# Performance work log

Hardware: AMD Instinct MI355X
Metric: run time of the kernel (lower is better)

## Reference

```python
import jax, jax.numpy as jnp
import numpy as np

N_NODES = 50000
IN_DIM = 128
HIDDEN = 64
OUT_DIM = 3
HEADS1 = 4
NEG_SLOPE = 0.2
EPS = 1e-16


def _glorot(key, shape):
    fan_in, fan_out = shape[0], shape[-1]
    lim = (6.0 / (fan_in + fan_out)) ** 0.5
    return jax.random.uniform(key, shape, jnp.float32, -lim, lim)


def setup_inputs() -> dict:
    key = jax.random.key(0)
    ks = jax.random.split(key, 12)
    x = jax.random.normal(ks[0], (N_NODES, IN_DIM), jnp.float32)
    edge_index = jax.random.randint(ks[1], (2, 400000), 0, N_NODES, jnp.int64)
    # layer 1: GATConv(in=128, out=64, heads=4)
    W1 = _glorot(ks[2], (IN_DIM, HEADS1 * HIDDEN))
    att_src1 = _glorot(ks[3], (HEADS1, HIDDEN))
    att_dst1 = _glorot(ks[4], (HEADS1, HIDDEN))
    b1 = jnp.zeros((HEADS1 * HIDDEN,), jnp.float32)
    # layer 2: GATConv(in=256, out=64, heads=1)
    W2 = _glorot(ks[5], (HEADS1 * HIDDEN, HIDDEN))
    att_src2 = _glorot(ks[6], (1, HIDDEN))
    att_dst2 = _glorot(ks[7], (1, HIDDEN))
    b2 = jnp.zeros((HIDDEN,), jnp.float32)
    # output linear
    Wout = _glorot(ks[8], (HIDDEN, OUT_DIM))
    bout = jnp.zeros((OUT_DIM,), jnp.float32)
    return {"x": x, "edge_index": edge_index, "W1": W1, "att_src1": att_src1,
            "att_dst1": att_dst1, "b1": b1, "W2": W2, "att_src2": att_src2,
            "att_dst2": att_dst2, "b2": b2, "Wout": Wout, "bout": bout}


def gat_conv(x, src, dst, W, a_src, a_dst, b, n_nodes):
    H, C = a_src.shape
    h = (x @ W).reshape(n_nodes, H, C)            # [N,H,C]
    a_s = jnp.sum(h * a_src[None], axis=-1)        # [N,H]
    a_d = jnp.sum(h * a_dst[None], axis=-1)        # [N,H]
    e = jax.nn.leaky_relu(a_s[src] + a_d[dst], NEG_SLOPE)  # [E,H]
    # segment softmax over incoming edges of each dst node
    m = jax.ops.segment_max(e, dst, num_segments=n_nodes)
    ex = jnp.exp(e - m[dst])
    denom = jax.ops.segment_sum(ex, dst, num_segments=n_nodes)
    alpha = ex / (denom[dst] + EPS)                # [E,H]
    msg = h[src] * alpha[..., None]                # [E,H,C]
    out = jax.ops.segment_sum(msg, dst, num_segments=n_nodes)
    return out.reshape(n_nodes, H * C) + b


def reference(x, edge_index, W1, att_src1, att_dst1, b1, W2, att_src2, att_dst2, b2, Wout, bout):
    n = x.shape[0]
    loop = jnp.arange(n, dtype=edge_index.dtype)
    src = jnp.concatenate([edge_index[0], loop])   # add self loops (PyG default)
    dst = jnp.concatenate([edge_index[1], loop])
    h = gat_conv(x, src, dst, W1, att_src1, att_dst1, b1, n)
    h = jax.nn.elu(h)
    h = gat_conv(h, src, dst, W2, att_src2, att_dst2, b2, n)
    h = jax.nn.elu(h)
    return h @ Wout + bout
```

## Files before the change

### kernel.cpp

```cpp
#include <hip/hip_runtime.h>
#include <hip/hip_bf16.h>
#include <math.h>

#define N_NODES  50000
#define IN_DIM   128
#define HIDDEN   64
#define OUT_DIM  3
#define HEADS1   4
#define E_RAW    400000
#define E_TOT    450000
#define NEG_SLOPE 0.2f
#define SCAN_CHUNK 1024
#define N_CHUNKS ((N_NODES + SCAN_CHUNK - 1) / SCAN_CHUNK)
#define WPREP_BLOCKS 128

typedef __attribute__((ext_vector_type(8))) short bf16x8;
typedef __attribute__((ext_vector_type(4))) float f32x4;

static __device__ __forceinline__ float bfu(unsigned short u) {
    return __uint_as_float(((unsigned)u) << 16);
}
static __device__ __forceinline__ unsigned short f2b_bits(float v) {
    __hip_bfloat16 b = __float2bfloat16(v);
    return *reinterpret_cast<unsigned short*>(&b);
}

static __device__ __forceinline__ void get_edge(const int* __restrict__ ei, int is64,
                                                int e, int& s, int& d) {
    if (e >= E_RAW) { s = d = e - E_RAW; return; }
    if (is64) { s = ei[2 * e]; d = ei[2 * E_RAW + 2 * e]; }
    else      { s = ei[e];     d = ei[E_RAW + e]; }
    s = min(max(s, 0), N_NODES - 1);
    d = min(max(d, 0), N_NODES - 1);
}

__global__ void detect_zero_kernel(const int* __restrict__ ei, int* __restrict__ flag,
                                   int* __restrict__ deg) {
    int gid = blockIdx.x * 256 + threadIdx.x;
    for (int i = gid; i < N_NODES; i += 64 * 256) deg[i] = 0;
    if (blockIdx.x == 0) {
        int nz = 0;
        #pragma unroll 4
        for (int t = 0; t < 32; t++) {
            int k = (threadIdx.x * 32 + t) * 48;
            nz |= ei[2 * k + 1];
        }
        __shared__ int s;
        if (threadIdx.x == 0) s = 0;
        __syncthreads();
        if (__any(nz != 0) && (threadIdx.x & 63) == 0) s = 1;
        __syncthreads();
        if (threadIdx.x == 0) flag[0] = s ? 0 : 1;
    }
}

__global__ void wprep_count_kernel(const float* __restrict__ W1, __hip_bfloat16* __restrict__ W1T,
                                   const float* __restrict__ W2, __hip_bfloat16* __restrict__ W2T,
                                   const int* __restrict__ ei, const int* __restrict__ flag,
                                   int* __restrict__ deg) {
    int bid = blockIdx.x;
    if (bid < WPREP_BLOCKS) {
        int i = bid * 256 + threadIdx.x;
        if (i < 256 * 128) {
            int n = i >> 7, k = i & 127;
            *((unsigned short*)W1T + i) = f2b_bits(W1[k * 256 + n]);
        }
        if (i < 64 * 256) {
            int n = i >> 8, k = i & 255;
            *((unsigned short*)W2T + i) = f2b_bits(W2[k * 64 + n]);
        }
        return;
    }
    int e = (bid - WPREP_BLOCKS) * 256 + threadIdx.x;
    if (e >= E_TOT) return;
    int s, d;
    get_edge(ei, flag[0], e, s, d);
    atomicAdd(&deg[d], 1);
}

__global__ void scan_local_kernel(const int* __restrict__ deg, int* __restrict__ row_ptr,
                                  int* __restrict__ bsums) {
    __shared__ int buf[SCAN_CHUNK];
    int base = blockIdx.x * SCAN_CHUNK;
    int i = base + threadIdx.x;
    buf[threadIdx.x] = (i < N_NODES) ? deg[i] : 0;
    __syncthreads();
    for (int off = 1; off < SCAN_CHUNK; off <<= 1) {
        int t = (threadIdx.x >= off) ? buf[threadIdx.x - off] : 0;
        __syncthreads();
        buf[threadIdx.x] += t;
        __syncthreads();
    }
    if (i < N_NODES) row_ptr[i + 1] = buf[threadIdx.x];
    if (threadIdx.x == SCAN_CHUNK - 1) bsums[blockIdx.x] = buf[SCAN_CHUNK - 1];
    if (blockIdx.x == 0 && threadIdx.x == 0) row_ptr[0] = 0;
}

__global__ void scan_add_kernel(int* __restrict__ row_ptr, const int* __restrict__ bsums,
                                const int* __restrict__ deg, int* __restrict__ cursor) {
    __shared__ int soff[64];
    if (threadIdx.x < 64) {
        int v = (threadIdx.x < N_CHUNKS) ? bsums[threadIdx.x] : 0;
        #pragma unroll
        for (int off = 1; off < 64; off <<= 1) {
            int t = __shfl_up(v, off, 64);
            if (threadIdx.x >= off) v += t;
        }
        soff[threadIdx.x] = v;
    }
    __syncthreads();
    int i = blockIdx.x * blockDim.x + threadIdx.x;
    if (i < N_NODES) {
        int ch = i / SCAN_CHUNK;
        int add = (ch == 0) ? 0 : soff[ch - 1];
        int incl = row_ptr[i + 1] + add;
        row_ptr[i + 1] = incl;
        cursor[i] = incl - deg[i];
    }
}

__global__ void scatter_kernel(const int* __restrict__ ei, const int* __restrict__ flag,
                               int* __restrict__ cursor, int* __restrict__ csr_src) {
    int e = blockIdx.x * blockDim.x + threadIdx.x;
    if (e >= E_TOT) return;
    int s, d;
    get_edge(ei, flag[0], e, s, d);
    int pos = atomicAdd(&cursor[d], 1);
    csr_src[pos] = s;
}

__global__ void __launch_bounds__(256) gemm_l1_mfma_kernel(
        const float* __restrict__ x, const __hip_bfloat16* __restrict__ W1T,
        const float* __restrict__ att_s, const float* __restrict__ att_d,
        __hip_bfloat16* __restrict__ h1,
        float* __restrict__ asb4, float* __restrict__ adb4) {
    __shared__ unsigned short As[16][136];
    const int tid = threadIdx.x;
    const int wave = tid >> 6, lane = tid & 63;
    const int quad = lane >> 4, m = lane & 15;
    const int row0 = blockIdx.x * 16;
    {
        int r = tid >> 4, seg = tid & 15;
        const float* xa = x + (size_t)(row0 + r) * IN_DIM + seg * 8;
        float4 u = *(const float4*)xa;
        float4 v = *(const float4*)(xa + 4);
        ushort4 p0, p1;
        p0.x = f2b_bits(u.x); p0.y = f2b_bits(u.y); p0.z = f2b_bits(u.z); p0.w = f2b_bits(u.w);
        p1.x = f2b_bits(v.x); p1.y = f2b_bits(v.y); p1.z = f2b_bits(v.z); p1.w = f2b_bits(v.w);
        *(ushort4*)&As[r][seg * 8]     = p0;
        *(ushort4*)&As[r][seg * 8 + 4] = p1;
    }
    __syncthreads();
    const int n0w = wave * 64;
    f32x4 acc0 = {0.f, 0.f, 0.f, 0.f}, acc1 = acc0, acc2 = acc0, acc3 = acc0;
    #pragma unroll
    for (int k0 = 0; k0 < IN_DIM; k0 += 32) {
        int kk = k0 + quad * 8;
        bf16x8 a = *(const bf16x8*)&As[m][kk];
        bf16x8 b0 = *(const bf16x8*)(W1T + (size_t)(n0w +  0 + m) * IN_DIM + kk);
        bf16x8 b1 = *(const bf16x8*)(W1T + (size_t)(n0w + 16 + m) * IN_DIM + kk);
        bf16x8 b2 = *(const bf16x8*)(W1T + (size_t)(n0w + 32 + m) * IN_DIM + kk);
        bf16x8 b3 = *(const bf16x8*)(W1T + (size_t)(n0w + 48 + m) * IN_DIM + kk);
        acc0 = __builtin_amdgcn_mfma_f32_16x16x32_bf16(a, b0, acc0, 0, 0, 0);
        acc1 = __builtin_amdgcn_mfma_f32_16x16x32_bf16(a, b1, acc1, 0, 0, 0);
        acc2 = __builtin_amdgcn_mfma_f32_16x16x32_bf16(a, b2, acc2, 0, 0, 0);
        acc3 = __builtin_amdgcn_mfma_f32_16x16x32_bf16(a, b3, acc3, 0, 0, 0);
    }
    float ats0 = att_s[n0w +  0 + m], atd0 = att_d[n0w +  0 + m];
    float ats1 = att_s[n0w + 16 + m], atd1 = att_d[n0w + 16 + m];
    float ats2 = att_s[n0w + 32 + m], atd2 = att_d[n0w + 32 + m];
    float ats3 = att_s[n0w + 48 + m], atd3 = att_d[n0w + 48 + m];
    unsigned short* out = (unsigned short*)h1;
    #pragma unroll
    for (int i = 0; i < 4; i++) {
        int grow = row0 + quad * 4 + i;
        size_t base = (size_t)grow * 256;
        out[base + n0w +  0 + m] = f2b_bits(acc0[i]);
        out[base + n0w + 16 + m] = f2b_bits(acc1[i]);
        out[base + n0w + 32 + m] = f2b_bits(acc2[i]);
        out[base + n0w + 48 + m] = f2b_bits(acc3[i]);
        float ps = acc0[i] * ats0 + acc1[i] * ats1 + acc2[i] * ats2 + acc3[i] * ats3;
        float pd = acc0[i] * atd0 + acc1[i] * atd1 + acc2[i] * atd2 + acc3[i] * atd3;
        #pragma unroll
        for (int off = 1; off < 16; off <<= 1) {
            ps += __shfl_xor(ps, off, 16);
            pd += __shfl_xor(pd, off, 16);
        }
        if (m == 0) {
            asb4[grow * 4 + wave] = ps;
            adb4[grow * 4 + wave] = pd;
        }
    }
}

__global__ void __launch_bounds__(256) gat_gather4_l2_kernel(
        const int* __restrict__ row_ptr, const int* __restrict__ csr_src,
        const float* __restrict__ asb4, const float* __restrict__ adb4,
        const __hip_bfloat16* __restrict__ h1, const float* __restrict__ bias,
        const __hip_bfloat16* __restrict__ W2T,
        const float* __restrict__ att_s, const float* __restrict__ att_d,
        __hip_bfloat16* __restrict__ h2,
        float* __restrict__ asb, float* __restrict__ adb) {
    __shared__ unsigned short As[16][264];
    __shared__ float sPS[4][16];
    __shared__ float sPD[4][16];
    const int tid = threadIdx.x;
    const int wave = tid >> 6, lane = tid & 63;
    const int row0 = blockIdx.x * 16;
    const int c    = lane & 31;
    const int slot = lane >> 5;
    const int head = c >> 3;
    const int eidx0 = lane >> 2;
    const int hh   = lane & 3;

    for (int g = 0; g < 4; g++) {
        const int n = row0 + wave * 4 + g;
        int b = row_ptr[n], e = row_ptr[n + 1];
        float adnh = adb4[n * 4 + hh];
        float acc[8];
        #pragma unroll
        for (int i = 0; i < 8; i++) acc[i] = 0.f;
        float l = 0.f;
        for (int c0 = b; c0 < e; c0 += 16) {
            int cnt = min(16, e - c0);
            int s_all = (lane < cnt) ? csr_src[c0 + lane] : 0;
            int sE = __shfl(s_all, eidx0, 64);
            float w_all = 0.f;
            if (eidx0 < cnt) {
                float v = asb4[sE * 4 + hh] + adnh;
                v = (v > 0.f) ? v : NEG_SLOPE * v;
                w_all = __expf(v);
            }
            #pragma unroll 2
            for (int k = 0; k < cnt; k += 2) {
                int eidx = k + slot;
                int s = __shfl(s_all, eidx, 64);
                float w = __shfl(w_all, eidx * 4 + head, 64);
                bf16x8 f = *(const bf16x8*)(h1 + (size_t)s * 256 + c * 8);
                l += w;
                #pragma unroll
                for (int i = 0; i < 8; i++)
                    acc[i] += w * bfu((unsigned short)f[i]);
            }
        }
        #pragma unroll
        for (int i = 0; i < 8; i++) acc[i] += __shfl_xor(acc[i], 32, 64);
        l += __shfl_xor(l, 32, 64);
        if (lane < 32) {
            float il = 1.f / (l + 1e-16f);
            float4 b0 = *(const float4*)(bias + c * 8);
            float4 b1 = *(const float4*)(bias + c * 8 + 4);
            float r[8];
            r[0] = acc[0] * il + b0.x; r[1] = acc[1] * il + b0.y;
            r[2] = acc[2] * il + b0.z; r[3] = acc[3] * il + b0.w;
            r[4] = acc[4] * il + b1.x; r[5] = acc[5] * il + b1.y;
            r[6] = acc[6] * il + b1.z; r[7] = acc[7] * il + b1.w;
            bf16x8 st;
            #pragma unroll
            for (int i = 0; i < 8; i++) {
                float v = (r[i] > 0.f) ? r[i] : expm1f(r[i]);
                st[i] = (short)f2b_bits(v);
            }
            *(bf16x8*)&As[wave * 4 + g][c * 8] = st;
        }
    }
    __syncthreads();

    const int quad = lane >> 4, m = lane & 15;
    const int n0 = wave * 16;
    f32x4 acc = {0.f, 0.f, 0.f, 0.f};
    #pragma unroll
    for (int k0 = 0; k0 < 256; k0 += 32) {
        int kk = k0 + quad * 8;
        bf16x8 a = *(const bf16x8*)&As[m][kk];
        bf16x8 bfr = *(const bf16x8*)(W2T + (size_t)(n0 + m) * 256 + kk);
        acc = __builtin_amdgcn_mfma_f32_16x16x32_bf16(a, bfr, acc, 0, 0, 0);
    }
    float ats = att_s[n0 + m], atd = att_d[n0 + m];
    unsigned short* out = (unsigned short*)h2;
    #pragma unroll
    for (int i = 0; i < 4; i++) {
        int grow = row0 + quad * 4 + i;
        out[(size_t)grow * 64 + n0 + m] = f2b_bits(acc[i]);
        float ps = acc[i] * ats;
        float pd = acc[i] * atd;
        #pragma unroll
        for (int off = 1; off < 16; off <<= 1) {
            ps += __shfl_xor(ps, off, 16);
            pd += __shfl_xor(pd, off, 16);
        }
        if (m == 0) {
            sPS[wave][quad * 4 + i] = ps;
            sPD[wave][quad * 4 + i] = pd;
        }
    }
    __syncthreads();
    if (tid < 16) {
        float ps = sPS[0][tid] + sPS[1][tid] + sPS[2][tid] + sPS[3][tid];
        float pd = sPD[0][tid] + sPD[1][tid] + sPD[2][tid] + sPD[3][tid];
        asb[row0 + tid] = ps;
        adb[row0 + tid] = pd;
    }
}

__global__ void __launch_bounds__(256) gat_gather1_out_kernel(
        const int* __restrict__ row_ptr, const int* __restrict__ csr_src,
        const float* __restrict__ asb, const float* __restrict__ adb,
        const __hip_bfloat16* __restrict__ h2, const float* __restrict__ bias,
        const float* __restrict__ Wout, const float* __restrict__ bout,
        float* __restrict__ out) {
    int wave = threadIdx.x >> 6;
    int lane = threadIdx.x & 63;
    int n = blockIdx.x * 4 + wave;
    if (n >= N_NODES) return;
    int b = row_ptr[n], e = row_ptr[n + 1];
    const int c    = lane & 7;
    const int slot = lane >> 3;
    float adn = adb[n];
    float acc[8];
    #pragma unroll
    for (int i = 0; i < 8; i++) acc[i] = 0.f;
    float l = 0.f;
    for (int c0 = b; c0 < e; c0 += 64) {
        int cnt = min(64, e - c0);
        int s_all = (lane < cnt) ? csr_src[c0 + lane] : 0;
        float w_all = 0.f;
        if (lane < cnt) {
            float v = asb[s_all] + adn;
            v = (v > 0.f) ? v : NEG_SLOPE * v;
            w_all = __expf(v);
        }
        #pragma unroll 2
        for (int k = 0; k < cnt; k += 8) {
            int eidx = k + slot;
            int s = __shfl(s_all, eidx, 64);
            float w = __shfl(w_all, eidx, 64);
            bf16x8 f = *(const bf16x8*)(h2 + (size_t)s * 64 + c * 8);
            l += w;
            #pragma unroll
            for (int i = 0; i < 8; i++)
                acc[i] += w * bfu((unsigned short)f[i]);
        }
    }
    #pragma unroll
    for (int off = 8; off < 64; off <<= 1) {
        #pragma unroll
        for (int i = 0; i < 8; i++) acc[i] += __shfl_xor(acc[i], off, 64);
        l += __shfl_xor(l, off, 64);
    }
    float il = 1.f / (l + 1e-16f);
    float4 b0 = *(const float4*)(bias + c * 8);
    float4 b1 = *(const float4*)(bias + c * 8 + 4);
    float v[8];
    v[0] = acc[0] * il + b0.x; v[1] = acc[1] * il + b0.y;
    v[2] = acc[2] * il + b0.z; v[3] = acc[3] * il + b0.w;
    v[4] = acc[4] * il + b1.x; v[5] = acc[5] * il + b1.y;
    v[6] = acc[6] * il + b1.z; v[7] = acc[7] * il + b1.w;
    #pragma unroll
    for (int i = 0; i < 8; i++) v[i] = (v[i] > 0.f) ? v[i] : expm1f(v[i]);
    const float* wp = Wout + c * 24;
    float o0 = 0.f, o1 = 0.f, o2 = 0.f;
    #pragma unroll
    for (int i = 0; i < 8; i++) {
        o0 += v[i] * wp[i * 3 + 0];
        o1 += v[i] * wp[i * 3 + 1];
        o2 += v[i] * wp[i * 3 + 2];
    }
    #pragma unroll
    for (int off = 1; off < 8; off <<= 1) {
        o0 += __shfl_xor(o0, off, 64);
        o1 += __shfl_xor(o1, off, 64);
        o2 += __shfl_xor(o2, off, 64);
    }
    if (lane == 0) {
        out[n * OUT_DIM + 0] = o0 + bout[0];
        out[n * OUT_DIM + 1] = o1 + bout[1];
        out[n * OUT_DIM + 2] = o2 + bout[2];
    }
}

extern "C" void kernel_launch(void* const* d_in, const int* in_sizes, int n_in,
                              void* d_out, int out_size, void* d_ws, size_t ws_size,
                              hipStream_t stream) {
    const float* x    = (const float*)d_in[0];
    const int*   ei   = (const int*)d_in[1];
    const float* W1   = (const float*)d_in[2];
    const float* as1  = (const float*)d_in[3];
    const float* ad1  = (const float*)d_in[4];
    const float* b1   = (const float*)d_in[5];
    const float* W2   = (const float*)d_in[6];
    const float* as2  = (const float*)d_in[7];
    const float* ad2  = (const float*)d_in[8];
    const float* b2v  = (const float*)d_in[9];
    const float* Wout = (const float*)d_in[10];
    const float* bout = (const float*)d_in[11];
    float* out = (float*)d_out;

    float* ws    = (float*)d_ws;
    int*   flag  = (int*)ws;
    float* asb4  = ws + 16;
    float* adb4  = asb4 + (size_t)N_NODES * 4;
    float* asb1  = adb4 + (size_t)N_NODES * 4;
    float* adb1  = asb1 + N_NODES;
    __hip_bfloat16* h1     = (__hip_bfloat16*)(adb1 + N_NODES);
    __hip_bfloat16* h2     = (__hip_bfloat16*)(h1 + (size_t)N_NODES * 256);
    __hip_bfloat16* W1T    = (__hip_bfloat16*)(h2 + (size_t)N_NODES * 64);
    __hip_bfloat16* W2T    = W1T + 256 * 128;
    int* deg     = (int*)(W2T + 64 * 256);
    int* bsums   = deg + N_NODES;
    int* row_ptr = bsums + 64;
    int* cursor  = row_ptr + N_NODES + 16;
    int* csr_src = cursor + N_NODES;

    const int EB = (E_TOT + 255) / 256;
    const int NB = (N_NODES + 255) / 256;
    const int AB = (N_NODES + 3) / 4;
    const int MB = N_NODES / 16;

    detect_zero_kernel<<<64, 256, 0, stream>>>(ei, flag, deg);
    wprep_count_kernel<<<WPREP_BLOCKS + EB, 256, 0, stream>>>(W1, W1T, W2, W2T, ei, flag, deg);
    scan_local_kernel<<<N_CHUNKS, SCAN_CHUNK, 0, stream>>>(deg, row_ptr, bsums);
    scan_add_kernel<<<NB, 256, 0, stream>>>(row_ptr, bsums, deg, cursor);
    scatter_kernel<<<EB, 256, 0, stream>>>(ei, flag, cursor, csr_src);

    gemm_l1_mfma_kernel<<<MB, 256, 0, stream>>>(x, W1T, as1, ad1, h1, asb4, adb4);

    gat_gather4_l2_kernel<<<MB, 256, 0, stream>>>(row_ptr, csr_src, asb4, adb4, h1, b1,
                                                  W2T, as2, ad2, h2, asb1, adb1);

    gat_gather1_out_kernel<<<AB, 256, 0, stream>>>(row_ptr, csr_src, asb1, adb1, h2,
                                                   b2v, Wout, bout, out);
}
```

Measured before the change: 267.7 us.

## Use one wave per node in layer-2 gather and rewrite local degree scan

The layer-2 gather kernel now launches 1024 threads per block, so each of 16 waves handles one destination node instead of each of 4 waves looping over four nodes. Only the first four waves then run the MFMA projection. This raises parallelism and latency hiding for the irregular gather, at the cost of larger blocks and idle waves during the GEMM phase. The local scan is replaced by a 256-thread, int4-per-thread wave-shuffle scan in place of a 1024-thread shared-memory Hillis-Steele scan. The int64-detect probe now reads 8192 contiguous indices in a coalesced pattern instead of a strided sample.

```diff
diff --git a/kernel.cpp b/kernel.cpp
--- a/kernel.cpp
+++ b/kernel.cpp
@@ -42,8 +42,8 @@
         int nz = 0;
         #pragma unroll 4
         for (int t = 0; t < 32; t++) {
-            int k = (threadIdx.x * 32 + t) * 48;
-            nz |= ei[2 * k + 1];
+            int i = t * 256 + threadIdx.x;
+            nz |= ei[2 * i + 1];
         }
         __shared__ int s;
         if (threadIdx.x == 0) s = 0;
@@ -80,20 +80,33 @@
 
 __global__ void scan_local_kernel(const int* __restrict__ deg, int* __restrict__ row_ptr,
                                   int* __restrict__ bsums) {
-    __shared__ int buf[SCAN_CHUNK];
-    int base = blockIdx.x * SCAN_CHUNK;
-    int i = base + threadIdx.x;
-    buf[threadIdx.x] = (i < N_NODES) ? deg[i] : 0;
+    __shared__ int wsum[4];
+    int t = threadIdx.x;
+    int wv = t >> 6, ln = t & 63;
+    int g = blockIdx.x * 256 + t;
+    int4 d = (g < 12500) ? ((const int4*)deg)[g] : make_int4(0, 0, 0, 0);
+    int p0 = d.x, p1 = p0 + d.y, p2 = p1 + d.z, p3 = p2 + d.w;
+    int s = p3;
+    #pragma unroll
+    for (int off = 1; off < 64; off <<= 1) {
+        int u = __shfl_up(s, off, 64);
+        if (ln >= off) s += u;
+    }
+    if (ln == 63) wsum[wv] = s;
     __syncthreads();
-    for (int off = 1; off < SCAN_CHUNK; off <<= 1) {
-        int t = (threadIdx.x >= off) ? buf[threadIdx.x - off] : 0;
-        __syncthreads();
-        buf[threadIdx.x] += t;
-        __syncthreads();
-    }
-    if (i < N_NODES) row_ptr[i + 1] = buf[threadIdx.x];
-    if (threadIdx.x == SCAN_CHUNK - 1) bsums[blockIdx.x] = buf[SCAN_CHUNK - 1];
-    if (blockIdx.x == 0 && threadIdx.x == 0) row_ptr[0] = 0;
+    int wbase = 0;
+    #pragma unroll
+    for (int w = 0; w < 4; w++) wbase += (w < wv) ? wsum[w] : 0;
+    int ex = wbase + s - p3;
+    if (g < 12500) {
+        int i = g * 4;
+        row_ptr[i + 1] = ex + p0;
+        row_ptr[i + 2] = ex + p1;
+        row_ptr[i + 3] = ex + p2;
+        row_ptr[i + 4] = ex + p3;
+    }
+    if (t == 255) bsums[blockIdx.x] = wbase + s;
+    if (blockIdx.x == 0 && t == 0) row_ptr[0] = 0;
 }
 
 __global__ void scan_add_kernel(int* __restrict__ row_ptr, const int* __restrict__ bsums,
@@ -193,7 +206,7 @@
     }
 }
 
-__global__ void __launch_bounds__(256) gat_gather4_l2_kernel(
+__global__ void __launch_bounds__(1024, 8) gat_gather4_l2_kernel(
         const int* __restrict__ row_ptr, const int* __restrict__ csr_src,
         const float* __restrict__ asb4, const float* __restrict__ adb4,
         const __hip_bfloat16* __restrict__ h1, const float* __restrict__ bias,
@@ -213,8 +226,8 @@
     const int eidx0 = lane >> 2;
     const int hh   = lane & 3;
 
-    for (int g = 0; g < 4; g++) {
-        const int n = row0 + wave * 4 + g;
+    {
+        const int n = row0 + wave;
         int b = row_ptr[n], e = row_ptr[n + 1];
         float adnh = adb4[n * 4 + hh];
         float acc[8];
@@ -261,37 +274,39 @@
                 float v = (r[i] > 0.f) ? r[i] : expm1f(r[i]);
                 st[i] = (short)f2b_bits(v);
             }
-            *(bf16x8*)&As[wave * 4 + g][c * 8] = st;
+            *(bf16x8*)&As[wave][c * 8] = st;
         }
     }
     __syncthreads();
 
-    const int quad = lane >> 4, m = lane & 15;
-    const int n0 = wave * 16;
-    f32x4 acc = {0.f, 0.f, 0.f, 0.f};
-    #pragma unroll
-    for (int k0 = 0; k0 < 256; k0 += 32) {
-        int kk = k0 + quad * 8;
-        bf16x8 a = *(const bf16x8*)&As[m][kk];
-        bf16x8 bfr = *(const bf16x8*)(W2T + (size_t)(n0 + m) * 256 + kk);
-        acc = __builtin_amdgcn_mfma_f32_16x16x32_bf16(a, bfr, acc, 0, 0, 0);
-    }
-    float ats = att_s[n0 + m], atd = att_d[n0 + m];
-    unsigned short* out = (unsigned short*)h2;
-    #pragma unroll
-    for (int i = 0; i < 4; i++) {
-        int grow = row0 + quad * 4 + i;
-        out[(size_t)grow * 64 + n0 + m] = f2b_bits(acc[i]);
-        float ps = acc[i] * ats;
-        float pd = acc[i] * atd;
-        #pragma unroll
-        for (int off = 1; off < 16; off <<= 1) {
-            ps += __shfl_xor(ps, off, 16);
-            pd += __shfl_xor(pd, off, 16);
-        }
-        if (m == 0) {
-            sPS[wave][quad * 4 + i] = ps;
-            sPD[wave][quad * 4 + i] = pd;
+    if (wave < 4) {
+        const int quad = lane >> 4, m = lane & 15;
+        const int n0 = wave * 16;
+        f32x4 acc = {0.f, 0.f, 0.f, 0.f};
+        #pragma unroll
+        for (int k0 = 0; k0 < 256; k0 += 32) {
+            int kk = k0 + quad * 8;
+            bf16x8 a = *(const bf16x8*)&As[m][kk];
+            bf16x8 bfr = *(const bf16x8*)(W2T + (size_t)(n0 + m) * 256 + kk);
+            acc = __builtin_amdgcn_mfma_f32_16x16x32_bf16(a, bfr, acc, 0, 0, 0);
+        }
+        float ats = att_s[n0 + m], atd = att_d[n0 + m];
+        unsigned short* out = (unsigned short*)h2;
+        #pragma unroll
+        for (int i = 0; i < 4; i++) {
+            int grow = row0 + quad * 4 + i;
+            out[(size_t)grow * 64 + n0 + m] = f2b_bits(acc[i]);
+            float ps = acc[i] * ats;
+            float pd = acc[i] * atd;
+            #pragma unroll
+            for (int off = 1; off < 16; off <<= 1) {
+                ps += __shfl_xor(ps, off, 16);
+                pd += __shfl_xor(pd, off, 16);
+            }
+            if (m == 0) {
+                sPS[wave][quad * 4 + i] = ps;
+                sPD[wave][quad * 4 + i] = pd;
+            }
         }
     }
     __syncthreads();
@@ -419,14 +434,14 @@
 
     detect_zero_kernel<<<64, 256, 0, stream>>>(ei, flag, deg);
     wprep_count_kernel<<<WPREP_BLOCKS + EB, 256, 0, stream>>>(W1, W1T, W2, W2T, ei, flag, deg);
-    scan_local_kernel<<<N_CHUNKS, SCAN_CHUNK, 0, stream>>>(deg, row_ptr, bsums);
+    scan_local_kernel<<<N_CHUNKS, 256, 0, stream>>>(deg, row_ptr, bsums);
     scan_add_kernel<<<NB, 256, 0, stream>>>(row_ptr, bsums, deg, cursor);
     scatter_kernel<<<EB, 256, 0, stream>>>(ei, flag, cursor, csr_src);
 
     gemm_l1_mfma_kernel<<<MB, 256, 0, stream>>>(x, W1T, as1, ad1, h1, asb4, adb4);
 
-    gat_gather4_l2_kernel<<<MB, 256, 0, stream>>>(row_ptr, csr_src, asb4, adb4, h1, b1,
-                                                  W2T, as2, ad2, h2, asb1, adb1);
+    gat_gather4_l2_kernel<<<MB, 1024, 0, stream>>>(row_ptr, csr_src, asb4, adb4, h1, b1,
+                                                   W2T, as2, ad2, h2, asb1, adb1);
 
     gat_gather1_out_kernel<<<AB, 256, 0, stream>>>(row_ptr, csr_src, asb1, adb1, h2,
                                                    b2v, Wout, bout, out);
```

New measurement: 263.9 us. No clear change (-1.4%).
